# Optimization experiments

Hardware: AMD Instinct MI355X
Metric: run time of the kernel (lower is better)

The kernel has to match this reference:

```python
import jax, jax.numpy as jnp
import numpy as np

N = 50000      # nodes
E = 800000     # edges (avg degree 16)
D = 64         # node_feature_dim
ED = 1         # edge_feature_dim
H = 128        # hidden_dim
G = 128        # graphs in batch
L = 3          # n_conv
EPS = 1e-5     # batchnorm eps


def setup_inputs() -> dict:
    key = jax.random.key(0)
    ks = jax.random.split(key, 20)
    w = lambda k, shp: (jax.random.normal(k, shp, dtype=jnp.float32)
                        / np.float32(np.sqrt(shp[-2] if len(shp) > 1 else 1.0)))
    return {
        "atom_z": jax.random.randint(ks[0], (N,), 0, 100),
        "edge_index": jax.random.randint(ks[1], (2, E), 0, N),
        "edge_attr": jax.random.normal(ks[2], (E, ED), dtype=jnp.float32),
        "batch": jnp.sort(jax.random.randint(ks[3], (N,), 0, G)),
        "emb": jax.random.normal(ks[4], (100, D), dtype=jnp.float32),
        "edge_W1": w(ks[5], (L, 2 * D + ED, H)), "edge_b1": jnp.zeros((L, H)),
        "edge_W2": w(ks[6], (L, H, H)),          "edge_b2": jnp.zeros((L, H)),
        "node_W1": w(ks[7], (L, D + H, H)),      "node_b1": jnp.zeros((L, H)),
        "node_W2": w(ks[8], (L, H, D)),          "node_b2": jnp.zeros((L, D)),
        "bn_gamma": jnp.ones((L, D)),            "bn_beta": jnp.zeros((L, D)),
        "out_W1": w(ks[9], (D, H)),  "out_b1": jnp.zeros((H,)),
        "out_W2": w(ks[10], (H, 1)), "out_b2": jnp.zeros((1,)),
    }


def reference(atom_z, edge_index, edge_attr, batch, emb,
              edge_W1, edge_b1, edge_W2, edge_b2,
              node_W1, node_b1, node_W2, node_b2,
              bn_gamma, bn_beta, out_W1, out_b1, out_W2, out_b2):
    sp = jax.nn.softplus
    src, dst = edge_index[0], edge_index[1]  # PyG source_to_target: x_j = x[src], x_i = x[dst]
    x = emb[atom_z]                          # [N, D]
    for l in range(L):
        # --- CGConv layer l ---
        z = jnp.concatenate([x[dst], x[src], edge_attr], axis=-1)        # [E, 2D+ED]
        m = sp(sp(z @ edge_W1[l] + edge_b1[l]) @ edge_W2[l] + edge_b2[l])  # [E, H]
        aggr = jax.ops.segment_sum(m, dst, num_segments=N)               # [N, H]
        h = jnp.concatenate([x, aggr], axis=-1)                          # [N, D+H]
        x = sp(h @ node_W1[l] + node_b1[l]) @ node_W2[l] + node_b2[l] + x
        # --- BatchNorm1d (training-mode batch stats) ---
        mu = jnp.mean(x, axis=0)
        var = jnp.mean(jnp.square(x - mu), axis=0)
        x = bn_gamma[l] * (x - mu) * jax.lax.rsqrt(var + EPS) + bn_beta[l]
    # --- global mean pool over graphs ---
    sums = jax.ops.segment_sum(x, batch, num_segments=G)                 # [G, D]
    cnts = jax.ops.segment_sum(jnp.ones((N, 1), x.dtype), batch, num_segments=G)
    pooled = sums / jnp.maximum(cnts, 1.0)
    # --- output MLP (dropout is identity at eval) ---
    out = sp(pooled @ out_W1 + out_b1) @ out_W2 + out_b2                 # [G, 1]
    return out
```

## Files before the change

### kernel.cpp

```cpp
#include <hip/hip_runtime.h>
#include <hip/hip_bf16.h>

#define N_NODES 50000
#define N_EDGES 800000
#define DIM 64
#define HID 128
#define NGRAPH 128
#define BN_EPS 1e-5f

typedef __attribute__((ext_vector_type(8))) short short8;
typedef __attribute__((ext_vector_type(4))) short short4v;
typedef __attribute__((ext_vector_type(4))) float f32x4;
typedef __attribute__((ext_vector_type(4))) int int4v;

__device__ __forceinline__ float sp_(float v) {
    return fmaxf(v, 0.f) + __logf(1.f + __expf(-fabsf(v)));
}
__device__ __forceinline__ short bfb(float f) {
    __hip_bfloat16 h = __float2bfloat16(f);
    return __builtin_bit_cast(short, h);
}
__device__ __forceinline__ float b2f(short s) {
    unsigned u = ((unsigned)(unsigned short)s) << 16;
    return __builtin_bit_cast(float, u);
}

__global__ void k_embed(const int* __restrict__ az, const float* __restrict__ emb,
                        float* __restrict__ x, __hip_bfloat16* __restrict__ xb) {
    int idx = blockIdx.x * 256 + threadIdx.x;
    if (idx >= N_NODES * DIM) return;
    int n = idx >> 6;
    int d = idx & 63;
    float v = emb[az[n] * DIM + d];
    x[idx] = v;
    xb[idx] = __float2bfloat16(v);
}

__global__ void k_wprep(const float* __restrict__ src, short* __restrict__ dst,
                        int total, int nshift, int srcStride) {
    int l = blockIdx.y;
    int idx = blockIdx.x * 256 + threadIdx.x;
    if (idx >= total) return;
    int K = total >> nshift;
    int k = idx >> nshift;
    int n = idx & ((1 << nshift) - 1);
    dst[(size_t)l * total + n * K + k] = bfb(src[(size_t)l * srcStride + idx]);
}

__global__ void k_hist(const int* __restrict__ edst, int* __restrict__ deg) {
    int e = blockIdx.x * 256 + threadIdx.x;
    if (e < N_EDGES) atomicAdd(&deg[edst[e]], 1);
}

__global__ void k_scan(const int* __restrict__ deg, int* __restrict__ cursor) {
    __shared__ int wsum[16];
    __shared__ int carry;
    const int t = threadIdx.x, lane = t & 63, w = t >> 6;
    if (t == 0) carry = 0;
    __syncthreads();
    for (int base = 0; base < N_NODES; base += 1024) {
        int i = base + t;
        int v = (i < N_NODES) ? deg[i] : 0;
        int s = v;
#pragma unroll
        for (int off = 1; off < 64; off <<= 1) {
            int u = __shfl_up(s, off);
            if (lane >= off) s += u;
        }
        if (lane == 63) wsum[w] = s;
        __syncthreads();
        if (w == 0) {
            int ws = (lane < 16) ? wsum[lane] : 0;
#pragma unroll
            for (int off = 1; off < 16; off <<= 1) {
                int u = __shfl_up(ws, off);
                if (lane >= off) ws += u;
            }
            if (lane < 16) wsum[lane] = ws;
        }
        __syncthreads();
        int woff = (w == 0) ? 0 : wsum[w - 1];
        int excl = carry + woff + s - v;
        if (i < N_NODES) cursor[i] = excl;
        __syncthreads();
        if (t == 1023) carry += wsum[15];
        __syncthreads();
    }
}

__global__ void k_scatter(const int* __restrict__ esrc, const int* __restrict__ edst,
                          const float* __restrict__ eattr, int* __restrict__ cursor,
                          int* __restrict__ ssrc, int* __restrict__ sdst,
                          float* __restrict__ sattr) {
    int e = blockIdx.x * 256 + threadIdx.x;
    if (e >= N_EDGES) return;
    int d = edst[e];
    int pos = atomicAdd(&cursor[d], 1);
    ssrc[pos] = esrc[e];
    sdst[pos] = d;
    sattr[pos] = eattr[e];
}

__global__ void k_gbounds(const int* __restrict__ batch, int* __restrict__ gstart) {
    int g = threadIdx.x;
    if (g > NGRAPH) return;
    int lo = 0, hi = N_NODES;
    while (lo < hi) {
        int mid = (lo + hi) >> 1;
        if (batch[mid] < g) lo = mid + 1; else hi = mid;
    }
    gstart[g] = lo;
}

__launch_bounds__(512, 2)
__global__ void k_ab(const __hip_bfloat16* __restrict__ xb,
                     const short* __restrict__ w1T, const float* __restrict__ b1,
                     short* __restrict__ xab) {
    __shared__ short xt[64 * 64];
    __shared__ short ot[64 * 256];
    const int t = threadIdx.x;
    const int wid = t >> 6, lane = t & 63, lrow = lane & 15, lk = lane >> 4;
    const int col = wid * 16 + lrow;
    const int n0 = blockIdx.x * 64;

    short8 wa[2], wb[2];
#pragma unroll
    for (int ks = 0; ks < 2; ks++) {
        wa[ks] = *(const short8*)((const char*)w1T + col * 256 + ks * 64 + lk * 16);
        wb[ks] = *(const short8*)((const char*)w1T + col * 256 + 128 + ks * 64 + lk * 16);
    }
    const float b1v = b1[col];

    {
        int r = t >> 3, q = t & 7;
        int node = n0 + r;
        int4v v = {0, 0, 0, 0};
        if (node < N_NODES) v = *(const int4v*)(xb + (size_t)node * DIM + q * 8);
        *(int4v*)((char*)xt + r * 128 + ((q * 16) ^ ((r & 7) << 4))) = v;
    }
    __syncthreads();

    f32x4 aa[4], ab[4];
#pragma unroll
    for (int mi = 0; mi < 4; mi++) { aa[mi] = (f32x4){0.f,0.f,0.f,0.f}; ab[mi] = (f32x4){0.f,0.f,0.f,0.f}; }
#pragma unroll
    for (int ks = 0; ks < 2; ks++) {
        int kb = ks * 64 + lk * 16;
        short8 av[4];
#pragma unroll
        for (int mi = 0; mi < 4; mi++) {
            int row = mi * 16 + lrow;
            av[mi] = *(const short8*)((const char*)xt + row * 128 + (kb ^ ((row & 7) << 4)));
        }
#pragma unroll
        for (int mi = 0; mi < 4; mi++) {
            aa[mi] = __builtin_amdgcn_mfma_f32_16x16x32_bf16(av[mi], wa[ks], aa[mi], 0, 0, 0);
            ab[mi] = __builtin_amdgcn_mfma_f32_16x16x32_bf16(av[mi], wb[ks], ab[mi], 0, 0, 0);
        }
    }
#pragma unroll
    for (int mi = 0; mi < 4; mi++) {
#pragma unroll
        for (int rr = 0; rr < 4; rr++) {
            int row = mi * 16 + lk * 4 + rr;
            int swz = (row & 7) << 4;
            *(short*)((char*)ot + row * 512 + ((col * 2) ^ swz)) = bfb(aa[mi][rr] + b1v);
            *(short*)((char*)ot + row * 512 + 256 + ((col * 2) ^ swz)) = bfb(ab[mi][rr]);
        }
    }
    __syncthreads();
#pragma unroll
    for (int it = 0; it < 4; it++) {
        int idx = it * 8192 + t * 16;
        int row = idx >> 9, off = idx & 511;
        int node = n0 + row;
        if (node < N_NODES) {
            int base = off & 256, lo = off & 255;
            int4v v = *(const int4v*)((char*)ot + row * 512 + base + (lo ^ ((row & 7) << 4)));
            *(int4v*)((char*)xab + (size_t)node * 512 + off) = v;
        }
    }
}

__launch_bounds__(512, 4)
__global__ void k_edge(const short* __restrict__ xab,
                       const int* __restrict__ ssrc, const int* __restrict__ sdst,
                       const float* __restrict__ sattr,
                       const float* __restrict__ wl, const float* __restrict__ b2,
                       const short* __restrict__ w2T,
                       float* __restrict__ aggr) {
    __shared__ short ht[64 * 128];
    __shared__ float mt[64 * 128];
    __shared__ int   dst_s[64];
    __shared__ int   seg_start[65];
    __shared__ int   seg_dst[64];
    __shared__ int   nseg_s;

    const int t = threadIdx.x;
    const int wid = t >> 6, lane = t & 63;
    const int lrow = lane & 15, lk = lane >> 4;
    const int r = t >> 3, q = t & 7;
    const int col = wid * 16 + lrow;

    short8 w2f[4];
#pragma unroll
    for (int ks = 0; ks < 4; ks++)
        w2f[ks] = *(const short8*)((const char*)w2T + col * 256 + ks * 64 + lk * 16);
    const float b2v = b2[col];
    float wlv[16];
#pragma unroll
    for (int i = 0; i < 16; i++) wlv[i] = wl[q * 16 + i];

    const int NT = N_EDGES / 64;
    const int tile0 = blockIdx.x * 25;
    const int tile1 = (tile0 + 25 < NT) ? tile0 + 25 : NT;

    for (int tile = tile0; tile < tile1; ++tile) {
        const int e0 = tile * 64;
        {
            int e = e0 + r;
            int dn = sdst[e], sn = ssrc[e];
            float at = sattr[e];
            if (q == 0) dst_s[r] = dn;
            const char* pa = (const char*)xab + (size_t)dn * 512 + q * 32;
            const char* pb = (const char*)xab + (size_t)sn * 512 + 256 + q * 32;
            short8 a0 = *(const short8*)pa, a1 = *(const short8*)(pa + 16);
            short8 b0 = *(const short8*)pb, b1x = *(const short8*)(pb + 16);
            short8 h0, h1;
#pragma unroll
            for (int i = 0; i < 8; i++) {
                h0[i] = bfb(sp_(b2f(a0[i]) + b2f(b0[i]) + at * wlv[i]));
                h1[i] = bfb(sp_(b2f(a1[i]) + b2f(b1x[i]) + at * wlv[8 + i]));
            }
            int swz = (r & 7) << 4;
            *(short8*)((char*)ht + r * 256 + ((q * 32) ^ swz)) = h0;
            *(short8*)((char*)ht + r * 256 + (((q * 32) + 16) ^ swz)) = h1;
        }
        __syncthreads();

        if (wid == 0) {
            int d = dst_s[lane];
            int prev = (lane == 0) ? -1 : dst_s[lane - 1];
            bool start = (d != prev);
            unsigned long long mask = __ballot(start);
            int sidx = __popcll(mask & ((1ull << lane) - 1));
            if (start) { seg_start[sidx] = lane; seg_dst[sidx] = d; }
            if (lane == 63) {
                int ns = __popcll(mask);
                nseg_s = ns;
                seg_start[ns] = 64;
            }
        }

        f32x4 acc2[4];
#pragma unroll
        for (int mi = 0; mi < 4; mi++) acc2[mi] = (f32x4){0.f, 0.f, 0.f, 0.f};
#pragma unroll
        for (int ks = 0; ks < 4; ks++) {
            int kb = ks * 64 + lk * 16;
            short8 av[4];
#pragma unroll
            for (int mi = 0; mi < 4; mi++) {
                int row = mi * 16 + lrow;
                av[mi] = *(const short8*)((const char*)ht + row * 256 + (kb ^ ((row & 7) << 4)));
            }
#pragma unroll
            for (int mi = 0; mi < 4; mi++)
                acc2[mi] = __builtin_amdgcn_mfma_f32_16x16x32_bf16(av[mi], w2f[ks], acc2[mi], 0, 0, 0);
        }
#pragma unroll
        for (int mi = 0; mi < 4; mi++) {
#pragma unroll
            for (int rr = 0; rr < 4; rr++) {
                int row = mi * 16 + lk * 4 + rr;
                *(float*)((char*)mt + row * 512 + ((col * 4) ^ ((row & 7) << 4))) = sp_(acc2[mi][rr] + b2v);
            }
        }
        __syncthreads();

        {
            int nseg = nseg_s;
            int rcol = t & 127, h = t >> 7;
            for (int s = h; s < nseg; s += 4) {
                int r0 = seg_start[s], r1 = seg_start[s + 1];
                float sum = 0.f;
                for (int rr = r0; rr < r1; rr++)
                    sum += *(const float*)((const char*)mt + rr * 512 + ((rcol * 4) ^ ((rr & 7) << 4)));
                atomicAdd(&aggr[(size_t)seg_dst[s] * HID + rcol], sum);
            }
        }
        __syncthreads();
    }
}

__launch_bounds__(256, 3)
__global__ void k_node(const __hip_bfloat16* __restrict__ xb,
                       const float* __restrict__ xf,
                       const float* __restrict__ aggr,
                       const short* __restrict__ w1T, const float* __restrict__ b1,
                       const short* __restrict__ w2T, const float* __restrict__ b2,
                       float* __restrict__ y, float* __restrict__ stats) {
    __shared__ short at[64 * 192];
    __shared__ short ht[64 * 128];

    const int t = threadIdx.x;
    const int wid = t >> 6, lane = t & 63, lrow = lane & 15, lk = lane >> 4;
    const int n0 = blockIdx.x * 64;

    const int nc0 = wid * 32;
    short8 w1f[6][2];
    float b1v[2];
#pragma unroll
    for (int ni = 0; ni < 2; ni++) {
        int col = nc0 + ni * 16 + lrow;
#pragma unroll
        for (int ks = 0; ks < 6; ks++) {
            int kb = ks * 64 + lk * 16;
            w1f[ks][ni] = *(const short8*)((const char*)w1T + col * 384 + kb);
        }
        b1v[ni] = b1[col];
    }
    const int nc2 = wid * 16;
    const int col2 = nc2 + lrow;
    short8 w2f[4];
#pragma unroll
    for (int ks = 0; ks < 4; ks++)
        w2f[ks] = *(const short8*)((const char*)w2T + col2 * 256 + ks * 64 + lk * 16);
    const float b2v = b2[col2];

    if (t < 64) {
        int node = n0 + t;
        if (node < N_NODES) {
            const __hip_bfloat16* xr = xb + (size_t)node * DIM;
#pragma unroll
            for (int i = 0; i < 8; i++) {
                int4v v = *(const int4v*)(xr + i * 8);
                *(int4v*)((char*)at + t * 384 + ((i * 16) ^ ((t & 7) << 4))) = v;
            }
        } else {
            int4v z = {0, 0, 0, 0};
#pragma unroll
            for (int i = 0; i < 8; i++)
                *(int4v*)((char*)at + t * 384 + ((i * 16) ^ ((t & 7) << 4))) = z;
        }
    }
    {
        int r = t >> 2, q = t & 3;
        int node = n0 + r;
#pragma unroll
        for (int i = 0; i < 4; i++) {
            short8 s = {0, 0, 0, 0, 0, 0, 0, 0};
            if (node < N_NODES) {
                const float* ar = aggr + (size_t)node * HID + q * 32 + i * 8;
                float4 f0 = *(const float4*)ar;
                float4 f1 = *(const float4*)(ar + 4);
                s = (short8){bfb(f0.x), bfb(f0.y), bfb(f0.z), bfb(f0.w),
                             bfb(f1.x), bfb(f1.y), bfb(f1.z), bfb(f1.w)};
            }
            int cb = 128 + q * 64 + i * 16;
            *(short8*)((char*)at + r * 384 + (cb ^ ((r & 7) << 4))) = s;
        }
    }
    __syncthreads();

    f32x4 acc[4][2];
#pragma unroll
    for (int mi = 0; mi < 4; mi++)
#pragma unroll
        for (int ni = 0; ni < 2; ni++) acc[mi][ni] = (f32x4){0.f, 0.f, 0.f, 0.f};
#pragma unroll
    for (int ks = 0; ks < 6; ks++) {
        int kb = ks * 64 + lk * 16;
        short8 av[4];
#pragma unroll
        for (int mi = 0; mi < 4; mi++) {
            int row = mi * 16 + lrow;
            av[mi] = *(const short8*)((const char*)at + row * 384 + (kb ^ ((row & 7) << 4)));
        }
#pragma unroll
        for (int mi = 0; mi < 4; mi++)
#pragma unroll
            for (int ni = 0; ni < 2; ni++)
                acc[mi][ni] = __builtin_amdgcn_mfma_f32_16x16x32_bf16(av[mi], w1f[ks][ni], acc[mi][ni], 0, 0, 0);
    }
#pragma unroll
    for (int mi = 0; mi < 4; mi++) {
#pragma unroll
        for (int ni = 0; ni < 2; ni++) {
            int col = nc0 + ni * 16 + lrow;
#pragma unroll
            for (int rr = 0; rr < 4; rr++) {
                int row = mi * 16 + lk * 4 + rr;
                float val = sp_(acc[mi][ni][rr] + b1v[ni]);
                *(short*)((char*)ht + row * 256 + ((col * 2) ^ ((row & 7) << 4))) = bfb(val);
            }
        }
    }
    __syncthreads();

    f32x4 acc2[4];
#pragma unroll
    for (int mi = 0; mi < 4; mi++) acc2[mi] = (f32x4){0.f, 0.f, 0.f, 0.f};
#pragma unroll
    for (int ks = 0; ks < 4; ks++) {
        int kb = ks * 64 + lk * 16;
        short8 av[4];
#pragma unroll
        for (int mi = 0; mi < 4; mi++) {
            int row = mi * 16 + lrow;
            av[mi] = *(const short8*)((const char*)ht + row * 256 + (kb ^ ((row & 7) << 4)));
        }
#pragma unroll
        for (int mi = 0; mi < 4; mi++)
            acc2[mi] = __builtin_amdgcn_mfma_f32_16x16x32_bf16(av[mi], w2f[ks], acc2[mi], 0, 0, 0);
    }
    float s1 = 0.f, s2 = 0.f;
#pragma unroll
    for (int mi = 0; mi < 4; mi++) {
#pragma unroll
        for (int rr = 0; rr < 4; rr++) {
            int row = mi * 16 + lk * 4 + rr;
            int node = n0 + row;
            if (node < N_NODES) {
                float v = acc2[mi][rr] + b2v + xf[(size_t)node * DIM + col2];
                y[(size_t)node * DIM + col2] = v;
                s1 += v;
                s2 += v * v;
            }
        }
    }
    s1 += __shfl_xor(s1, 16); s1 += __shfl_xor(s1, 32);
    s2 += __shfl_xor(s2, 16); s2 += __shfl_xor(s2, 32);
    if (lane < 16) {
        atomicAdd(&stats[col2], s1);
        atomicAdd(&stats[64 + col2], s2);
    }
}

__global__ void k_bnfin(const float* __restrict__ gamma, const float* __restrict__ beta,
                        float* __restrict__ stats) {
    int d = threadIdx.x;
    float mu = stats[d] * (1.f / N_NODES);
    float var = stats[64 + d] * (1.f / N_NODES) - mu * mu;
    float rstd = rsqrtf(var + BN_EPS);
    float a = gamma[d] * rstd;
    stats[128 + d] = a;
    stats[192 + d] = beta[d] - mu * a;
}

__global__ void k_bnapply(const float* __restrict__ y, const float* __restrict__ stats,
                          float* __restrict__ x, __hip_bfloat16* __restrict__ xb) {
    int idx = (blockIdx.x * 256 + threadIdx.x) * 4;
    if (idx >= N_NODES * DIM) return;
    int d = idx & 63;
    float4 v = *(const float4*)(y + idx);
    float4 r;
    r.x = stats[128 + d + 0] * v.x + stats[192 + d + 0];
    r.y = stats[128 + d + 1] * v.y + stats[192 + d + 1];
    r.z = stats[128 + d + 2] * v.z + stats[192 + d + 2];
    r.w = stats[128 + d + 3] * v.w + stats[192 + d + 3];
    *(float4*)(x + idx) = r;
    short4v s = {bfb(r.x), bfb(r.y), bfb(r.z), bfb(r.w)};
    *(short4v*)((char*)(xb + idx)) = s;
}

__global__ void k_pool2(const int* __restrict__ gstart, const float* __restrict__ x,
                        float* __restrict__ pooled) {
    __shared__ float red[256];
    const int g = blockIdx.x, t = threadIdx.x;
    const int d = t & 63, nl = t >> 6;
    const int s = gstart[g], e = gstart[g + 1];
    float sum = 0.f;
    for (int n = s + nl; n < e; n += 4)
        sum += x[(size_t)n * DIM + d];
    red[t] = sum;
    __syncthreads();
    if (t < 64) {
        float tot = red[t] + red[t + 64] + red[t + 128] + red[t + 192];
        int c = e - s;
        pooled[g * DIM + t] = tot / fmaxf((float)c, 1.f);
    }
}

__global__ void k_out(const float* __restrict__ pooled,
                      const float* __restrict__ W1, const float* __restrict__ b1,
                      const float* __restrict__ W2, const float* __restrict__ b2,
                      float* __restrict__ out) {
    __shared__ float pl[64];
    __shared__ float wsum[2];
    int g = blockIdx.x, t = threadIdx.x;
    if (t < 64) pl[t] = pooled[g * 64 + t];
    __syncthreads();
    float a = b1[t];
#pragma unroll
    for (int d = 0; d < 64; d++) a += pl[d] * W1[d * 128 + t];
    float c = sp_(a) * W2[t];
#pragma unroll
    for (int off = 32; off >= 1; off >>= 1) c += __shfl_down(c, off);
    int lane = t & 63, wid = t >> 6;
    if (lane == 0) wsum[wid] = c;
    __syncthreads();
    if (t == 0) out[g] = wsum[0] + wsum[1] + b2[0];
}

extern "C" void kernel_launch(void* const* d_in, const int* in_sizes, int n_in,
                              void* d_out, int out_size, void* d_ws, size_t ws_size,
                              hipStream_t stream) {
    const int*   az    = (const int*)d_in[0];
    const int*   ei    = (const int*)d_in[1];
    const float* eattr = (const float*)d_in[2];
    const int*   batch = (const int*)d_in[3];
    const float* emb   = (const float*)d_in[4];
    const float* eW1   = (const float*)d_in[5];
    const float* eb1   = (const float*)d_in[6];
    const float* eW2   = (const float*)d_in[7];
    const float* eb2   = (const float*)d_in[8];
    const float* nW1   = (const float*)d_in[9];
    const float* nb1   = (const float*)d_in[10];
    const float* nW2   = (const float*)d_in[11];
    const float* nb2   = (const float*)d_in[12];
    const float* gam   = (const float*)d_in[13];
    const float* bet   = (const float*)d_in[14];
    const float* oW1   = (const float*)d_in[15];
    const float* ob1   = (const float*)d_in[16];
    const float* oW2   = (const float*)d_in[17];
    const float* ob2   = (const float*)d_in[18];
    const int* esrc = ei;
    const int* edst = ei + N_EDGES;

    float* x     = (float*)d_ws;
    float* y     = x + (size_t)N_NODES * DIM;
    float* aggr  = y + (size_t)N_NODES * DIM;
    float* stats = aggr + (size_t)N_NODES * HID;
    float* pooled = stats + 256;
    __hip_bfloat16* xb = (__hip_bfloat16*)(pooled + NGRAPH * DIM);
    short* ew1T = (short*)(xb + (size_t)N_NODES * DIM);
    short* ew2T = ew1T + 3 * 128 * 128;
    short* nw1T = ew2T + 3 * 128 * 128;
    short* nw2T = nw1T + 3 * 128 * 192;
    int*   cursor = (int*)(nw2T + 3 * 64 * 128);
    int*   ssrc   = cursor + N_NODES;
    int*   sdstA  = ssrc + N_EDGES;
    float* sattr  = (float*)(sdstA + N_EDGES);
    int*   gstart = (int*)(sattr + N_EDGES);
    short* xab    = (short*)(gstart + 256);

    k_embed<<<(N_NODES * DIM + 255) / 256, 256, 0, stream>>>(az, emb, x, xb);

    k_wprep<<<dim3(64, 3), 256, 0, stream>>>(eW1, ew1T, 128 * 128, 7, 129 * 128);
    k_wprep<<<dim3(64, 3), 256, 0, stream>>>(eW2, ew2T, 128 * 128, 7, 128 * 128);
    k_wprep<<<dim3(96, 3), 256, 0, stream>>>(nW1, nw1T, 192 * 128, 7, 192 * 128);
    k_wprep<<<dim3(32, 3), 256, 0, stream>>>(nW2, nw2T, 128 * 64, 6, 128 * 64);

    hipMemsetAsync(cursor, 0, N_NODES * sizeof(int), stream);
    k_hist<<<(N_EDGES + 255) / 256, 256, 0, stream>>>(edst, cursor);
    k_scan<<<1, 1024, 0, stream>>>(cursor, cursor);
    k_scatter<<<(N_EDGES + 255) / 256, 256, 0, stream>>>(esrc, edst, eattr, cursor,
                                                         ssrc, sdstA, sattr);
    k_gbounds<<<1, 256, 0, stream>>>(batch, gstart);

    for (int l = 0; l < 3; l++) {
        hipMemsetAsync(aggr, 0, ((size_t)N_NODES * HID + 256) * sizeof(float), stream);
        k_ab<<<(N_NODES + 63) / 64, 512, 0, stream>>>(xb, ew1T + (size_t)l * 128 * 128,
                                                      eb1 + l * 128, xab);
        k_edge<<<500, 512, 0, stream>>>(xab, ssrc, sdstA, sattr,
                                        eW1 + (size_t)l * 129 * 128 + 128 * 128,
                                        eb2 + l * 128,
                                        ew2T + (size_t)l * 128 * 128,
                                        aggr);
        k_node<<<(N_NODES + 63) / 64, 256, 0, stream>>>(xb, x, aggr,
                                                        nw1T + (size_t)l * 128 * 192, nb1 + l * 128,
                                                        nw2T + (size_t)l * 64 * 128, nb2 + l * 64,
                                                        y, stats);
        k_bnfin<<<1, 64, 0, stream>>>(gam + l * 64, bet + l * 64, stats);
        k_bnapply<<<(N_NODES * DIM / 4 + 255) / 256, 256, 0, stream>>>(y, stats, x, xb);
    }

    k_pool2<<<NGRAPH, 256, 0, stream>>>(gstart, x, pooled);
    k_out<<<NGRAPH, 128, 0, stream>>>(pooled, oW1, ob1, oW2, ob2, (float*)d_out);
}
```

Before: 977.5 us.

## Pack sorted edge records and software-prefetch next edge tile gathers

Packs src, dst and edge attribute into one 16-byte record per sorted edge so each edge is fetched with a single vector load. The edge kernel now loads the next tile's record and gathered node rows into registers during the current tile's aggregation, overlapping gather latency with compute. It also removes the trailing barrier per tile and doubles the block count with balanced tile ranges. The cost is more register pressure and a slightly larger edge buffer.

```diff
diff --git a/kernel.cpp b/kernel.cpp
--- a/kernel.cpp
+++ b/kernel.cpp
@@ -90,15 +90,13 @@
 
 __global__ void k_scatter(const int* __restrict__ esrc, const int* __restrict__ edst,
                           const float* __restrict__ eattr, int* __restrict__ cursor,
-                          int* __restrict__ ssrc, int* __restrict__ sdst,
-                          float* __restrict__ sattr) {
+                          int4v* __restrict__ sedge) {
     int e = blockIdx.x * 256 + threadIdx.x;
     if (e >= N_EDGES) return;
     int d = edst[e];
     int pos = atomicAdd(&cursor[d], 1);
-    ssrc[pos] = esrc[e];
-    sdst[pos] = d;
-    sattr[pos] = eattr[e];
+    int4v rec = {esrc[e], d, __builtin_bit_cast(int, eattr[e]), 0};
+    sedge[pos] = rec;
 }
 
 __global__ void k_gbounds(const int* __restrict__ batch, int* __restrict__ gstart) {
@@ -184,8 +182,7 @@
 
 __launch_bounds__(512, 4)
 __global__ void k_edge(const short* __restrict__ xab,
-                       const int* __restrict__ ssrc, const int* __restrict__ sdst,
-                       const float* __restrict__ sattr,
+                       const int4v* __restrict__ sedge,
                        const float* __restrict__ wl, const float* __restrict__ b2,
                        const short* __restrict__ w2T,
                        float* __restrict__ aggr) {
@@ -212,25 +209,29 @@
     for (int i = 0; i < 16; i++) wlv[i] = wl[q * 16 + i];
 
     const int NT = N_EDGES / 64;
-    const int tile0 = blockIdx.x * 25;
-    const int tile1 = (tile0 + 25 < NT) ? tile0 + 25 : NT;
+    const int tile0 = (int)(((long)blockIdx.x * NT) / 1000);
+    const int tile1 = (int)(((long)(blockIdx.x + 1) * NT) / 1000);
+
+    int4v ei;
+    short8 ra0, ra1, rb0, rb1;
+    {
+        int e = tile0 * 64 + r;
+        ei = sedge[e];
+        const char* pa = (const char*)xab + (size_t)ei[1] * 512 + q * 32;
+        const char* pb = (const char*)xab + (size_t)ei[0] * 512 + 256 + q * 32;
+        ra0 = *(const short8*)pa;  ra1 = *(const short8*)(pa + 16);
+        rb0 = *(const short8*)pb;  rb1 = *(const short8*)(pb + 16);
+    }
 
     for (int tile = tile0; tile < tile1; ++tile) {
-        const int e0 = tile * 64;
         {
-            int e = e0 + r;
-            int dn = sdst[e], sn = ssrc[e];
-            float at = sattr[e];
-            if (q == 0) dst_s[r] = dn;
-            const char* pa = (const char*)xab + (size_t)dn * 512 + q * 32;
-            const char* pb = (const char*)xab + (size_t)sn * 512 + 256 + q * 32;
-            short8 a0 = *(const short8*)pa, a1 = *(const short8*)(pa + 16);
-            short8 b0 = *(const short8*)pb, b1x = *(const short8*)(pb + 16);
+            float at = __builtin_bit_cast(float, ei[2]);
+            if (q == 0) dst_s[r] = ei[1];
             short8 h0, h1;
 #pragma unroll
             for (int i = 0; i < 8; i++) {
-                h0[i] = bfb(sp_(b2f(a0[i]) + b2f(b0[i]) + at * wlv[i]));
-                h1[i] = bfb(sp_(b2f(a1[i]) + b2f(b1x[i]) + at * wlv[8 + i]));
+                h0[i] = bfb(sp_(b2f(ra0[i]) + b2f(rb0[i]) + at * wlv[i]));
+                h1[i] = bfb(sp_(b2f(ra1[i]) + b2f(rb1[i]) + at * wlv[8 + i]));
             }
             int swz = (r & 7) << 4;
             *(short8*)((char*)ht + r * 256 + ((q * 32) ^ swz)) = h0;
@@ -278,6 +279,15 @@
         }
         __syncthreads();
 
+        if (tile + 1 < tile1) {
+            int e = (tile + 1) * 64 + r;
+            ei = sedge[e];
+            const char* pa = (const char*)xab + (size_t)ei[1] * 512 + q * 32;
+            const char* pb = (const char*)xab + (size_t)ei[0] * 512 + 256 + q * 32;
+            ra0 = *(const short8*)pa;  ra1 = *(const short8*)(pa + 16);
+            rb0 = *(const short8*)pb;  rb1 = *(const short8*)(pb + 16);
+        }
+
         {
             int nseg = nseg_s;
             int rcol = t & 127, h = t >> 7;
@@ -289,7 +299,6 @@
                 atomicAdd(&aggr[(size_t)seg_dst[s] * HID + rcol], sum);
             }
         }
-        __syncthreads();
     }
 }
 
@@ -539,10 +548,8 @@
     short* nw1T = ew2T + 3 * 128 * 128;
     short* nw2T = nw1T + 3 * 128 * 192;
     int*   cursor = (int*)(nw2T + 3 * 64 * 128);
-    int*   ssrc   = cursor + N_NODES;
-    int*   sdstA  = ssrc + N_EDGES;
-    float* sattr  = (float*)(sdstA + N_EDGES);
-    int*   gstart = (int*)(sattr + N_EDGES);
+    int4v* sedge  = (int4v*)(cursor + N_NODES + 48);
+    int*   gstart = (int*)(sedge + N_EDGES);
     short* xab    = (short*)(gstart + 256);
 
     k_embed<<<(N_NODES * DIM + 255) / 256, 256, 0, stream>>>(az, emb, x, xb);
@@ -555,19 +562,18 @@
     hipMemsetAsync(cursor, 0, N_NODES * sizeof(int), stream);
     k_hist<<<(N_EDGES + 255) / 256, 256, 0, stream>>>(edst, cursor);
     k_scan<<<1, 1024, 0, stream>>>(cursor, cursor);
-    k_scatter<<<(N_EDGES + 255) / 256, 256, 0, stream>>>(esrc, edst, eattr, cursor,
-                                                         ssrc, sdstA, sattr);
+    k_scatter<<<(N_EDGES + 255) / 256, 256, 0, stream>>>(esrc, edst, eattr, cursor, sedge);
     k_gbounds<<<1, 256, 0, stream>>>(batch, gstart);
 
     for (int l = 0; l < 3; l++) {
         hipMemsetAsync(aggr, 0, ((size_t)N_NODES * HID + 256) * sizeof(float), stream);
         k_ab<<<(N_NODES + 63) / 64, 512, 0, stream>>>(xb, ew1T + (size_t)l * 128 * 128,
                                                       eb1 + l * 128, xab);
-        k_edge<<<500, 512, 0, stream>>>(xab, ssrc, sdstA, sattr,
-                                        eW1 + (size_t)l * 129 * 128 + 128 * 128,
-                                        eb2 + l * 128,
-                                        ew2T + (size_t)l * 128 * 128,
-                                        aggr);
+        k_edge<<<1000, 512, 0, stream>>>(xab, sedge,
+                                         eW1 + (size_t)l * 129 * 128 + 128 * 128,
+                                         eb2 + l * 128,
+                                         ew2T + (size_t)l * 128 * 128,
+                                         aggr);
         k_node<<<(N_NODES + 63) / 64, 256, 0, stream>>>(xb, x, aggr,
                                                         nw1T + (size_t)l * 128 * 192, nb1 + l * 128,
                                                         nw2T + (size_t)l * 64 * 128, nb2 + l * 64,
```

Result: faster. 956.7 us (-2.1%).
